# Kernel optimization log

Measured on AMD Instinct MI355X. Metric: run time of the kernel, lower is better.

## Reference

```python
import jax, jax.numpy as jnp
import numpy as np

OMEGA = 30.0
B = 65536
NUM_FREQ = 8  # int(base_dim / in_features) = 32 / 4


def _siren_w(k, out_dim, in_dim, first=False):
    bound = (1.0 / in_dim) if first else (np.sqrt(6.0 / in_dim) / OMEGA)
    return jax.random.uniform(k, (out_dim, in_dim), jnp.float32, -bound, bound)


def _lin_w(k, out_dim, in_dim):
    bound = np.sqrt(1.0 / in_dim)
    return jax.random.uniform(k, (out_dim, in_dim), jnp.float32, -bound, bound)


def setup_inputs() -> dict:
    key = jax.random.key(0)
    ks = jax.random.split(key, 16)
    E = 7
    d = {}
    d['x'] = jax.random.uniform(ks[0], (B, 4), jnp.float32, -1.0, 1.0)
    # encoder: pos_dim=64 -> sine1(128) -> sine2(256) -> resblock(256, bottleneck 128)
    d['enc_s1_w'] = _siren_w(ks[1], 128, 64, first=True); d['enc_s1_b'] = jnp.zeros((128,), jnp.float32)
    d['enc_s2_w'] = _siren_w(ks[2], 256, 128); d['enc_s2_b'] = jnp.zeros((256,), jnp.float32)
    d['res_fc1_w'] = _lin_w(ks[3], 128, 256); d['res_fc1_b'] = jnp.zeros((128,), jnp.float32)
    d['res_fc2_w'] = _lin_w(ks[4], 128, 128); d['res_fc2_b'] = jnp.zeros((128,), jnp.float32)
    d['res_fc3_w'] = _lin_w(ks[5], 256, 128); d['res_fc3_b'] = jnp.zeros((256,), jnp.float32)
    # policy: 4 -> 128 (first sine) -> 128 (sine); gate in = 256+128=384 -> 7
    d['pol_s1_w'] = _siren_w(ks[6], 128, 4, first=True); d['pol_s1_b'] = jnp.zeros((128,), jnp.float32)
    d['pol_s2_w'] = _siren_w(ks[7], 128, 128); d['pol_s2_b'] = jnp.zeros((128,), jnp.float32)
    d['gate_w'] = _siren_w(ks[8], 7, 384); d['gate_b'] = jnp.zeros((7,), jnp.float32)
    # 7 experts: SirenMLP 256 -> 256 (first sine) -> 256 (sine) -> final Linear 256 -> 1
    bnd1 = 1.0 / 256.0
    d['exp_s1_w'] = jax.random.uniform(ks[9], (E, 256, 256), jnp.float32, -bnd1, bnd1)
    d['exp_s1_b'] = jnp.zeros((E, 256), jnp.float32)
    bnd2 = np.sqrt(6.0 / 256.0) / OMEGA
    d['exp_s2_w'] = jax.random.uniform(ks[10], (E, 256, 256), jnp.float32, -bnd2, bnd2)
    d['exp_s2_b'] = jnp.zeros((E, 256), jnp.float32)
    d['exp_fin_w'] = jax.random.uniform(ks[11], (E, 1, 256), jnp.float32, -bnd2, bnd2)
    d['exp_fin_b'] = jnp.zeros((E, 1), jnp.float32)
    return d


def reference(x, enc_s1_w, enc_s1_b, enc_s2_w, enc_s2_b, res_fc1_w, res_fc1_b,
              res_fc2_w, res_fc2_b, res_fc3_w, res_fc3_b, pol_s1_w, pol_s1_b,
              pol_s2_w, pol_s2_b, gate_w, gate_b, exp_s1_w, exp_s1_b,
              exp_s2_w, exp_s2_b, exp_fin_w, exp_fin_b):
    # NeRF-style positional encoding: log-sampled freqs, no include_input
    freqs = (2.0 ** jnp.arange(NUM_FREQ, dtype=jnp.float32)) * jnp.pi  # [F]
    ang = x[:, :, None] * freqs                                        # [B,4,F]
    pe = jnp.concatenate([jnp.sin(ang), jnp.cos(ang)], axis=-1)        # [B,4,2F]
    pe = pe.reshape(x.shape[0], -1)                                    # [B,64]
    # shared encoder: sine1 -> sine2 -> bottleneck res block
    h = jnp.sin(OMEGA * (pe @ enc_s1_w.T + enc_s1_b))                  # [B,128]
    h = jnp.sin(OMEGA * (h @ enc_s2_w.T + enc_s2_b))                   # [B,256]
    r = jax.nn.relu(h @ res_fc1_w.T + res_fc1_b)                       # [B,128]
    r = jax.nn.relu(r @ res_fc2_w.T + res_fc2_b)                       # [B,128]
    r = r @ res_fc3_w.T + res_fc3_b                                    # [B,256]
    enc_feat = jax.nn.relu(r + h)                                      # [B,256]
    # policy: sine feature net + gate over [enc_feat, pol_feat]
    pf = jnp.sin(OMEGA * (x @ pol_s1_w.T + pol_s1_b))                  # [B,128]
    pf = jnp.sin(OMEGA * (pf @ pol_s2_w.T + pol_s2_b))                 # [B,128]
    logits = jnp.concatenate([enc_feat, pf], axis=-1) @ gate_w.T + gate_b  # [B,7]
    probs = jax.nn.softmax(logits, axis=-1)                            # [B,7]
    # all 7 expert SIREN MLPs as batched GEMMs over expert axis e
    e = jnp.sin(OMEGA * (jnp.einsum('bd,eod->beo', enc_feat, exp_s1_w) + exp_s1_b))  # [B,7,256]
    e = jnp.sin(OMEGA * (jnp.einsum('beh,eoh->beo', e, exp_s2_w) + exp_s2_b))        # [B,7,256]
    preds = jnp.einsum('beh,eoh->beo', e, exp_fin_w) + exp_fin_b                     # [B,7,1]
    # soft routing: probability-weighted combination
    y = jnp.sum(preds * probs[:, :, None], axis=1)                     # [B,1]
    return y
```

## Files before the change

### kernel.cpp

```cpp
#include <hip/hip_runtime.h>


typedef short v8s __attribute__((ext_vector_type(8)));
typedef float v4f __attribute__((ext_vector_type(4)));

#define KSIN 4.774648293f
#define AST 264
#define PST 9
#define N_CVT 8

__device__ __forceinline__ float bf2f(unsigned short h) {
  union { unsigned u; float f; } v; v.u = ((unsigned)h) << 16; return v.f;
}
__device__ __forceinline__ unsigned short f2bf(float f) {
  union { float f; unsigned u; } v; v.f = f;
  unsigned r = v.u + 0x7fffu + ((v.u >> 16) & 1u);
  return (unsigned short)(r >> 16);
}
__device__ __forceinline__ unsigned pack2(float a, float b) {
  return (unsigned)f2bf(a) | ((unsigned)f2bf(b) << 16);
}
__device__ __forceinline__ float sin_rev(float x) {
  return __builtin_amdgcn_sinf(x);
}
__device__ __forceinline__ float cos_rev(float x) {
  return __builtin_amdgcn_cosf(x);
}

struct CvtArgs {
  const float* src[N_CVT];
  unsigned     off[N_CVT];
  unsigned     n[N_CVT];
  float        scl[N_CVT];
};

__global__ void convert_kernel(CvtArgs a, unsigned short* __restrict__ dst) {
  const int tid = blockIdx.x * blockDim.x + threadIdx.x;
  const int stride = gridDim.x * blockDim.x;
  for (int k = 0; k < N_CVT; k++) {
    const unsigned n4 = a.n[k] >> 2;
    const float4* s = (const float4*)a.src[k];
    const float sc = a.scl[k];
    uint2* d = (uint2*)(dst + a.off[k]);
    for (unsigned i = tid; i < n4; i += stride) {
      float4 v = s[i];
      uint2 o; o.x = pack2(v.x * sc, v.y * sc); o.y = pack2(v.z * sc, v.w * sc);
      d[i] = o;
    }
    for (unsigned i = (n4 << 2) + tid; i < a.n[k]; i += stride)
      dst[a.off[k] + i] = f2bf(a.src[k][i] * sc);
  }
}

template<int K, int NPW, int ACT>
__device__ __forceinline__ void wgemm(const unsigned short* A,
                                      unsigned short* OUT, int oc,
                                      const unsigned short* __restrict__ W,
                                      const float* __restrict__ bias,
                                      const unsigned short* skip) {
  const int lane = threadIdx.x & 63;
  const int wave = threadIdx.x >> 6;
  const int m15  = lane & 15;
  const int q    = lane >> 4;
  const int n0   = wave * (NPW * 16);
  v4f acc[NPW][4];
#pragma unroll
  for (int i = 0; i < NPW; i++)
#pragma unroll
    for (int j = 0; j < 4; j++) acc[i][j] = (v4f){0.f, 0.f, 0.f, 0.f};

#pragma unroll
  for (int k0 = 0; k0 < K / 32; ++k0) {
    v8s a[4], b[NPW];
#pragma unroll
    for (int rt = 0; rt < 4; rt++)
      a[rt] = *(const v8s*)(A + (rt * 16 + m15) * AST + k0 * 32 + q * 8);
#pragma unroll
    for (int ct = 0; ct < NPW; ct++)
      b[ct] = *(const v8s*)(W + (size_t)(n0 + ct * 16 + m15) * K + k0 * 32 + q * 8);
#pragma unroll
    for (int ct = 0; ct < NPW; ct++)
#pragma unroll
      for (int rt = 0; rt < 4; rt++)
        acc[ct][rt] = __builtin_amdgcn_mfma_f32_16x16x32_bf16(b[ct], a[rt], acc[ct][rt], 0, 0, 0);
  }

#pragma unroll
  for (int ct = 0; ct < NPW; ct++) {
    const int c0 = n0 + ct * 16 + q * 4;
    v4f bv = *(const v4f*)(bias + c0);
    if (ACT == 0) bv *= KSIN;
#pragma unroll
    for (int rt = 0; rt < 4; rt++) {
      const int row = rt * 16 + m15;
      float o0, o1, o2, o3;
      if (ACT == 2) {
        const uint2 sk = *(const uint2*)(skip + row * AST + c0);
        o0 = fmaxf(acc[ct][rt][0] + bv[0] + bf2f((unsigned short)(sk.x & 0xffffu)), 0.f);
        o1 = fmaxf(acc[ct][rt][1] + bv[1] + bf2f((unsigned short)(sk.x >> 16)), 0.f);
        o2 = fmaxf(acc[ct][rt][2] + bv[2] + bf2f((unsigned short)(sk.y & 0xffffu)), 0.f);
        o3 = fmaxf(acc[ct][rt][3] + bv[3] + bf2f((unsigned short)(sk.y >> 16)), 0.f);
      } else if (ACT == 1) {
        o0 = fmaxf(acc[ct][rt][0] + bv[0], 0.f);
        o1 = fmaxf(acc[ct][rt][1] + bv[1], 0.f);
        o2 = fmaxf(acc[ct][rt][2] + bv[2], 0.f);
        o3 = fmaxf(acc[ct][rt][3] + bv[3], 0.f);
      } else {
        o0 = sin_rev(acc[ct][rt][0] + bv[0]);
        o1 = sin_rev(acc[ct][rt][1] + bv[1]);
        o2 = sin_rev(acc[ct][rt][2] + bv[2]);
        o3 = sin_rev(acc[ct][rt][3] + bv[3]);
      }
      uint2 w2; w2.x = pack2(o0, o1); w2.y = pack2(o2, o3);
      *(uint2*)(OUT + row * AST + oc + c0) = w2;
    }
  }
}

__device__ __forceinline__ void wexpert2(const unsigned short* A,
                                         const unsigned short* __restrict__ W,
                                         const float* __restrict__ bias,
                                         const float* __restrict__ wfin,
                                         float* __restrict__ pred_part) {
  const int lane = threadIdx.x & 63;
  const int wave = threadIdx.x >> 6;
  const int m15  = lane & 15;
  const int q    = lane >> 4;
  const int n0   = wave * 32;
  v4f acc[2][4];
#pragma unroll
  for (int i = 0; i < 2; i++)
#pragma unroll
    for (int j = 0; j < 4; j++) acc[i][j] = (v4f){0.f, 0.f, 0.f, 0.f};

#pragma unroll
  for (int k0 = 0; k0 < 8; ++k0) {
    v8s a[4], b[2];
#pragma unroll
    for (int rt = 0; rt < 4; rt++)
      a[rt] = *(const v8s*)(A + (rt * 16 + m15) * AST + k0 * 32 + q * 8);
#pragma unroll
    for (int ct = 0; ct < 2; ct++)
      b[ct] = *(const v8s*)(W + (size_t)(n0 + ct * 16 + m15) * 256 + k0 * 32 + q * 8);
#pragma unroll
    for (int ct = 0; ct < 2; ct++)
#pragma unroll
      for (int rt = 0; rt < 4; rt++)
        acc[ct][rt] = __builtin_amdgcn_mfma_f32_16x16x32_bf16(b[ct], a[rt], acc[ct][rt], 0, 0, 0);
  }

  float p[4] = {0.f, 0.f, 0.f, 0.f};
#pragma unroll
  for (int ct = 0; ct < 2; ct++) {
    const int c0 = n0 + ct * 16 + q * 4;
    v4f bv = *(const v4f*)(bias + c0);
    bv *= KSIN;
    const v4f wf = *(const v4f*)(wfin + c0);
#pragma unroll
    for (int rt = 0; rt < 4; rt++)
#pragma unroll
      for (int r = 0; r < 4; r++)
        p[rt] += sin_rev(acc[ct][rt][r] + bv[r]) * wf[r];
  }
#pragma unroll
  for (int rt = 0; rt < 4; rt++) {
    float v = p[rt];
    v += __shfl_xor(v, 16);
    v += __shfl_xor(v, 32);
    if (q == 0) pred_part[wave * 64 + rt * 16 + m15] = v;
  }
}

__global__ __launch_bounds__(512, 2) void moe_inr_kernel(
    const float* __restrict__ x,
    const unsigned short* __restrict__ es1w, const float* __restrict__ es1b,
    const unsigned short* __restrict__ es2w, const float* __restrict__ es2b,
    const unsigned short* __restrict__ rf1w, const float* __restrict__ rf1b,
    const unsigned short* __restrict__ rf2w, const float* __restrict__ rf2b,
    const unsigned short* __restrict__ rf3w, const float* __restrict__ rf3b,
    const float* __restrict__ ps1w,          const float* __restrict__ ps1b,
    const unsigned short* __restrict__ ps2w, const float* __restrict__ ps2b,
    const float* __restrict__ gw,            const float* __restrict__ gb,
    const unsigned short* __restrict__ xs1w, const float* __restrict__ xs1b,
    const unsigned short* __restrict__ xs2w, const float* __restrict__ xs2b,
    const float* __restrict__ xfw,           const float* __restrict__ xfb,
    float* __restrict__ out) {
  __shared__ __align__(16) unsigned short P[2][64 * AST];
  __shared__ __align__(16) unsigned short Q[2][64 * AST];
  __shared__ float probs[2][64 * PST];
  __shared__ float pred_part[2][8 * 64];

  const int t   = threadIdx.x;
  const int r0g = blockIdx.x * 128;

#pragma unroll
  for (int tl = 0; tl < 2; ++tl) {
    const int row = t & 63, g = t >> 6, c = g & 3, jh = g >> 2;
    const float xv = x[(r0g + tl * 64 + row) * 4 + c];
    float sn[4], cs[4];
#pragma unroll
    for (int jj = 0; jj < 4; jj++) {
      const int j = jh * 4 + jj;
      const float rev = xv * (0.5f * (float)(1 << j));
      sn[jj] = sin_rev(rev);
      cs[jj] = cos_rev(rev);
    }
    uint2 ws; ws.x = pack2(sn[0], sn[1]); ws.y = pack2(sn[2], sn[3]);
    uint2 wc2; wc2.x = pack2(cs[0], cs[1]); wc2.y = pack2(cs[2], cs[3]);
    *(uint2*)(P[tl] + row * AST + c * 16 + jh * 4) = ws;
    *(uint2*)(P[tl] + row * AST + c * 16 + 8 + jh * 4) = wc2;
  }
  __syncthreads();
  wgemm<64, 1, 0>(P[0], P[0], 64, es1w, es1b, nullptr);
  wgemm<64, 1, 0>(P[1], P[1], 64, es1w, es1b, nullptr);
  __syncthreads();
  wgemm<128, 2, 0>(P[0] + 64, Q[0], 0, es2w, es2b, nullptr);
  wgemm<128, 2, 0>(P[1] + 64, Q[1], 0, es2w, es2b, nullptr);
  __syncthreads();
  wgemm<256, 1, 1>(Q[0], P[0], 0, rf1w, rf1b, nullptr);
  wgemm<256, 1, 1>(Q[1], P[1], 0, rf1w, rf1b, nullptr);
  __syncthreads();
  wgemm<128, 1, 1>(P[0], P[0], 128, rf2w, rf2b, nullptr);
  wgemm<128, 1, 1>(P[1], P[1], 128, rf2w, rf2b, nullptr);
  __syncthreads();
  wgemm<128, 2, 2>(P[0] + 128, Q[0], 0, rf3w, rf3b, Q[0]);
  wgemm<128, 2, 2>(P[1] + 128, Q[1], 0, rf3w, rf3b, Q[1]);
  __syncthreads();
#pragma unroll
  for (int tl = 0; tl < 2; ++tl) {
    const int row = t & 63, g = t >> 6;
    const v4f xv = *(const v4f*)(x + (r0g + tl * 64 + row) * 4);
#pragma unroll
    for (int ii = 0; ii < 4; ii++) {
      float oo[4];
#pragma unroll
      for (int i2 = 0; i2 < 4; i2++) {
        const int o = g * 16 + ii * 4 + i2;
        const v4f w4 = *(const v4f*)(ps1w + o * 4);
        const float z = xv[0] * w4[0] + xv[1] * w4[1] + xv[2] * w4[2] +
                        xv[3] * w4[3] + ps1b[o];
        oo[i2] = sin_rev(KSIN * z);
      }
      uint2 w2; w2.x = pack2(oo[0], oo[1]); w2.y = pack2(oo[2], oo[3]);
      *(uint2*)(P[tl] + row * AST + g * 16 + ii * 4) = w2;
    }
  }
  __syncthreads();
  wgemm<128, 1, 0>(P[0], P[0], 128, ps2w, ps2b, nullptr);
  wgemm<128, 1, 0>(P[1], P[1], 128, ps2w, ps2b, nullptr);
  __syncthreads();
#pragma unroll
  for (int tl = 0; tl < 2; ++tl) {
    const int row = t >> 3, pp = t & 7;
    float lg[7] = {0.f, 0.f, 0.f, 0.f, 0.f, 0.f, 0.f};
#pragma unroll
    for (int u = 0; u < 6; u++) {
      const int kk = pp * 48 + u * 8;
      const v8s av = (kk < 256) ? *(const v8s*)(Q[tl] + row * AST + kk)
                                : *(const v8s*)(P[tl] + row * AST + 128 + (kk - 256));
      float af[8];
#pragma unroll
      for (int e2 = 0; e2 < 8; e2++) af[e2] = bf2f((unsigned short)av[e2]);
#pragma unroll
      for (int j = 0; j < 7; j++) {
        const v4f g0 = *(const v4f*)(gw + j * 384 + kk);
        const v4f g1 = *(const v4f*)(gw + j * 384 + kk + 4);
        lg[j] += af[0] * g0[0] + af[1] * g0[1] + af[2] * g0[2] + af[3] * g0[3] +
                 af[4] * g1[0] + af[5] * g1[1] + af[6] * g1[2] + af[7] * g1[3];
      }
    }
#pragma unroll
    for (int j = 0; j < 7; j++) {
      float s = lg[j];
      s += __shfl_xor(s, 1);
      s += __shfl_xor(s, 2);
      s += __shfl_xor(s, 4);
      lg[j] = s;
    }
    if (pp == 0) {
#pragma unroll
      for (int j = 0; j < 7; j++) probs[tl][row * PST + j] = lg[j] + gb[j];
    }
  }
  __syncthreads();
  float yr = 0.f;
  if (t < 128) {
    const int tl = t >> 6, row = t & 63;
    float m = probs[tl][row * PST];
#pragma unroll
    for (int j = 1; j < 7; j++) m = fmaxf(m, probs[tl][row * PST + j]);
    float s = 0.f, e[7];
#pragma unroll
    for (int j = 0; j < 7; j++) { e[j] = __expf(probs[tl][row * PST + j] - m); s += e[j]; }
    const float inv = 1.f / s;
#pragma unroll
    for (int j = 0; j < 7; j++) probs[tl][row * PST + j] = e[j] * inv;
  }
  for (int ex = 0; ex < 7; ++ex) {
    wgemm<256, 2, 0>(Q[0], P[0], 0, xs1w + ex * 65536, xs1b + ex * 256, nullptr);
    wgemm<256, 2, 0>(Q[1], P[1], 0, xs1w + ex * 65536, xs1b + ex * 256, nullptr);
    __syncthreads();
    wexpert2(P[0], xs2w + ex * 65536, xs2b + ex * 256, xfw + ex * 256, pred_part[0]);
    wexpert2(P[1], xs2w + ex * 65536, xs2b + ex * 256, xfw + ex * 256, pred_part[1]);
    __syncthreads();
    if (t < 128) {
      const int tl = t >> 6, row = t & 63;
      float pr = 0.f;
#pragma unroll
      for (int w = 0; w < 8; w++) pr += pred_part[tl][w * 64 + row];
      yr += (pr + xfb[ex]) * probs[tl][row * PST + ex];
    }
  }
  if (t < 128) out[r0g + t] = yr;
}

extern "C" void kernel_launch(void* const* d_in, const int* in_sizes, int n_in,
                              void* d_out, int out_size, void* d_ws, size_t ws_size,
                              hipStream_t stream) {
  (void)out_size; (void)n_in; (void)ws_size;
  const int   idx[N_CVT] = {1, 3, 5, 7, 9, 13, 17, 19};
  const float scl[N_CVT] = {KSIN, KSIN, 1.f, 1.f, 1.f, KSIN, KSIN, KSIN};
  unsigned off[N_CVT], cur = 0;
  CvtArgs a;
  for (int i = 0; i < N_CVT; i++) {
    off[i] = cur;
    a.src[i] = (const float*)d_in[idx[i]];
    a.off[i] = cur;
    a.n[i]   = (unsigned)in_sizes[idx[i]];
    a.scl[i] = scl[i];
    cur += ((unsigned)in_sizes[idx[i]] + 7u) & ~7u;
  }
  unsigned short* dst = (unsigned short*)d_ws;
  hipLaunchKernelGGL(convert_kernel, dim3(1024), dim3(256), 0, stream, a, dst);
  hipLaunchKernelGGL(moe_inr_kernel, dim3(65536 / 128), dim3(512), 0, stream,
      (const float*)d_in[0],
      dst + off[0], (const float*)d_in[2],
      dst + off[1], (const float*)d_in[4],
      dst + off[2], (const float*)d_in[6],
      dst + off[3], (const float*)d_in[8],
      dst + off[4], (const float*)d_in[10],
      (const float*)d_in[11], (const float*)d_in[12],
      dst + off[5], (const float*)d_in[14],
      (const float*)d_in[15], (const float*)d_in[16],
      dst + off[6], (const float*)d_in[18],
      dst + off[7], (const float*)d_in[20],
      (const float*)d_in[21], (const float*)d_in[22],
      (float*)d_out);
}
```

Before: 350.3 us.

## Split waves across the two row tiles instead of looping tiles per wave

Each GEMM stage now assigns half the waves (4 of 8) to each 64-row tile, with every wave covering twice as many output columns, instead of every wave processing both tiles one after the other. Each wave loads its weight fragments once and reuses them across 4 column tiles, which cuts global weight traffic per wave and removes the serial tile loop. In exchange each wave holds more accumulator registers (up to 16 v4f), which raises register pressure under the 512x2 launch bounds and may cause spills.

```diff
diff --git a/kernel.cpp b/kernel.cpp
--- a/kernel.cpp
+++ b/kernel.cpp
@@ -53,16 +53,24 @@
 }
 
 template<int K, int NPW, int ACT>
-__device__ __forceinline__ void wgemm(const unsigned short* A,
-                                      unsigned short* OUT, int oc,
-                                      const unsigned short* __restrict__ W,
-                                      const float* __restrict__ bias,
-                                      const unsigned short* skip) {
+__device__ __forceinline__ void wgemm1(const unsigned short* A0,
+                                       const unsigned short* A1,
+                                       unsigned short* O0, unsigned short* O1,
+                                       int oc,
+                                       const unsigned short* __restrict__ W,
+                                       const float* __restrict__ bias,
+                                       const unsigned short* skip0,
+                                       const unsigned short* skip1) {
   const int lane = threadIdx.x & 63;
   const int wave = threadIdx.x >> 6;
+  const int tl   = wave >> 2;
+  const int wl   = wave & 3;
   const int m15  = lane & 15;
   const int q    = lane >> 4;
-  const int n0   = wave * (NPW * 16);
+  const int n0   = wl * (NPW * 16);
+  const unsigned short* A   = tl ? A1 : A0;
+  unsigned short*       OUT = tl ? O1 : O0;
+  const unsigned short* skp = tl ? skip1 : skip0;
   v4f acc[NPW][4];
 #pragma unroll
   for (int i = 0; i < NPW; i++)
@@ -73,11 +81,11 @@
   for (int k0 = 0; k0 < K / 32; ++k0) {
     v8s a[4], b[NPW];
 #pragma unroll
+    for (int ct = 0; ct < NPW; ct++)
+      b[ct] = *(const v8s*)(W + (size_t)(n0 + ct * 16 + m15) * K + k0 * 32 + q * 8);
+#pragma unroll
     for (int rt = 0; rt < 4; rt++)
       a[rt] = *(const v8s*)(A + (rt * 16 + m15) * AST + k0 * 32 + q * 8);
-#pragma unroll
-    for (int ct = 0; ct < NPW; ct++)
-      b[ct] = *(const v8s*)(W + (size_t)(n0 + ct * 16 + m15) * K + k0 * 32 + q * 8);
 #pragma unroll
     for (int ct = 0; ct < NPW; ct++)
 #pragma unroll
@@ -93,23 +101,24 @@
 #pragma unroll
     for (int rt = 0; rt < 4; rt++) {
       const int row = rt * 16 + m15;
+      const v4f av = acc[ct][rt];
       float o0, o1, o2, o3;
       if (ACT == 2) {
-        const uint2 sk = *(const uint2*)(skip + row * AST + c0);
-        o0 = fmaxf(acc[ct][rt][0] + bv[0] + bf2f((unsigned short)(sk.x & 0xffffu)), 0.f);
-        o1 = fmaxf(acc[ct][rt][1] + bv[1] + bf2f((unsigned short)(sk.x >> 16)), 0.f);
-        o2 = fmaxf(acc[ct][rt][2] + bv[2] + bf2f((unsigned short)(sk.y & 0xffffu)), 0.f);
-        o3 = fmaxf(acc[ct][rt][3] + bv[3] + bf2f((unsigned short)(sk.y >> 16)), 0.f);
+        const uint2 sk = *(const uint2*)(skp + row * AST + c0);
+        o0 = fmaxf(av[0] + bv[0] + bf2f((unsigned short)(sk.x & 0xffffu)), 0.f);
+        o1 = fmaxf(av[1] + bv[1] + bf2f((unsigned short)(sk.x >> 16)), 0.f);
+        o2 = fmaxf(av[2] + bv[2] + bf2f((unsigned short)(sk.y & 0xffffu)), 0.f);
+        o3 = fmaxf(av[3] + bv[3] + bf2f((unsigned short)(sk.y >> 16)), 0.f);
       } else if (ACT == 1) {
-        o0 = fmaxf(acc[ct][rt][0] + bv[0], 0.f);
-        o1 = fmaxf(acc[ct][rt][1] + bv[1], 0.f);
-        o2 = fmaxf(acc[ct][rt][2] + bv[2], 0.f);
-        o3 = fmaxf(acc[ct][rt][3] + bv[3], 0.f);
+        o0 = fmaxf(av[0] + bv[0], 0.f);
+        o1 = fmaxf(av[1] + bv[1], 0.f);
+        o2 = fmaxf(av[2] + bv[2], 0.f);
+        o3 = fmaxf(av[3] + bv[3], 0.f);
       } else {
-        o0 = sin_rev(acc[ct][rt][0] + bv[0]);
-        o1 = sin_rev(acc[ct][rt][1] + bv[1]);
-        o2 = sin_rev(acc[ct][rt][2] + bv[2]);
-        o3 = sin_rev(acc[ct][rt][3] + bv[3]);
+        o0 = sin_rev(av[0] + bv[0]);
+        o1 = sin_rev(av[1] + bv[1]);
+        o2 = sin_rev(av[2] + bv[2]);
+        o3 = sin_rev(av[3] + bv[3]);
       }
       uint2 w2; w2.x = pack2(o0, o1); w2.y = pack2(o2, o3);
       *(uint2*)(OUT + row * AST + oc + c0) = w2;
@@ -117,33 +126,37 @@
   }
 }
 
-__device__ __forceinline__ void wexpert2(const unsigned short* A,
-                                         const unsigned short* __restrict__ W,
-                                         const float* __restrict__ bias,
-                                         const float* __restrict__ wfin,
-                                         float* __restrict__ pred_part) {
+__device__ __forceinline__ void wexpert2s(const unsigned short* A0,
+                                          const unsigned short* A1,
+                                          const unsigned short* __restrict__ W,
+                                          const float* __restrict__ bias,
+                                          const float* __restrict__ wfin,
+                                          float* __restrict__ pp) {
   const int lane = threadIdx.x & 63;
   const int wave = threadIdx.x >> 6;
+  const int tl   = wave >> 2;
+  const int wl   = wave & 3;
   const int m15  = lane & 15;
   const int q    = lane >> 4;
-  const int n0   = wave * 32;
-  v4f acc[2][4];
-#pragma unroll
-  for (int i = 0; i < 2; i++)
+  const int n0   = wl * 64;
+  const unsigned short* A = tl ? A1 : A0;
+  v4f acc[4][4];
+#pragma unroll
+  for (int i = 0; i < 4; i++)
 #pragma unroll
     for (int j = 0; j < 4; j++) acc[i][j] = (v4f){0.f, 0.f, 0.f, 0.f};
 
 #pragma unroll
   for (int k0 = 0; k0 < 8; ++k0) {
-    v8s a[4], b[2];
+    v8s a[4], b[4];
+#pragma unroll
+    for (int ct = 0; ct < 4; ct++)
+      b[ct] = *(const v8s*)(W + (size_t)(n0 + ct * 16 + m15) * 256 + k0 * 32 + q * 8);
 #pragma unroll
     for (int rt = 0; rt < 4; rt++)
       a[rt] = *(const v8s*)(A + (rt * 16 + m15) * AST + k0 * 32 + q * 8);
 #pragma unroll
-    for (int ct = 0; ct < 2; ct++)
-      b[ct] = *(const v8s*)(W + (size_t)(n0 + ct * 16 + m15) * 256 + k0 * 32 + q * 8);
-#pragma unroll
-    for (int ct = 0; ct < 2; ct++)
+    for (int ct = 0; ct < 4; ct++)
 #pragma unroll
       for (int rt = 0; rt < 4; rt++)
         acc[ct][rt] = __builtin_amdgcn_mfma_f32_16x16x32_bf16(b[ct], a[rt], acc[ct][rt], 0, 0, 0);
@@ -151,7 +164,7 @@
 
   float p[4] = {0.f, 0.f, 0.f, 0.f};
 #pragma unroll
-  for (int ct = 0; ct < 2; ct++) {
+  for (int ct = 0; ct < 4; ct++) {
     const int c0 = n0 + ct * 16 + q * 4;
     v4f bv = *(const v4f*)(bias + c0);
     bv *= KSIN;
@@ -167,7 +180,7 @@
     float v = p[rt];
     v += __shfl_xor(v, 16);
     v += __shfl_xor(v, 32);
-    if (q == 0) pred_part[wave * 64 + rt * 16 + m15] = v;
+    if (q == 0) pp[tl * 256 + wl * 64 + rt * 16 + m15] = v;
   }
 }
 
@@ -188,7 +201,7 @@
   __shared__ __align__(16) unsigned short P[2][64 * AST];
   __shared__ __align__(16) unsigned short Q[2][64 * AST];
   __shared__ float probs[2][64 * PST];
-  __shared__ float pred_part[2][8 * 64];
+  __shared__ float pred_part[2 * 4 * 64];
 
   const int t   = threadIdx.x;
   const int r0g = blockIdx.x * 128;
@@ -211,20 +224,15 @@
     *(uint2*)(P[tl] + row * AST + c * 16 + 8 + jh * 4) = wc2;
   }
   __syncthreads();
-  wgemm<64, 1, 0>(P[0], P[0], 64, es1w, es1b, nullptr);
-  wgemm<64, 1, 0>(P[1], P[1], 64, es1w, es1b, nullptr);
-  __syncthreads();
-  wgemm<128, 2, 0>(P[0] + 64, Q[0], 0, es2w, es2b, nullptr);
-  wgemm<128, 2, 0>(P[1] + 64, Q[1], 0, es2w, es2b, nullptr);
-  __syncthreads();
-  wgemm<256, 1, 1>(Q[0], P[0], 0, rf1w, rf1b, nullptr);
-  wgemm<256, 1, 1>(Q[1], P[1], 0, rf1w, rf1b, nullptr);
-  __syncthreads();
-  wgemm<128, 1, 1>(P[0], P[0], 128, rf2w, rf2b, nullptr);
-  wgemm<128, 1, 1>(P[1], P[1], 128, rf2w, rf2b, nullptr);
-  __syncthreads();
-  wgemm<128, 2, 2>(P[0] + 128, Q[0], 0, rf3w, rf3b, Q[0]);
-  wgemm<128, 2, 2>(P[1] + 128, Q[1], 0, rf3w, rf3b, Q[1]);
+  wgemm1<64, 2, 0>(P[0], P[1], P[0], P[1], 64, es1w, es1b, nullptr, nullptr);
+  __syncthreads();
+  wgemm1<128, 4, 0>(P[0] + 64, P[1] + 64, Q[0], Q[1], 0, es2w, es2b, nullptr, nullptr);
+  __syncthreads();
+  wgemm1<256, 2, 1>(Q[0], Q[1], P[0], P[1], 0, rf1w, rf1b, nullptr, nullptr);
+  __syncthreads();
+  wgemm1<128, 2, 1>(P[0], P[1], P[0], P[1], 128, rf2w, rf2b, nullptr, nullptr);
+  __syncthreads();
+  wgemm1<128, 4, 2>(P[0] + 128, P[1] + 128, Q[0], Q[1], 0, rf3w, rf3b, Q[0], Q[1]);
   __syncthreads();
 #pragma unroll
   for (int tl = 0; tl < 2; ++tl) {
@@ -246,8 +254,7 @@
     }
   }
   __syncthreads();
-  wgemm<128, 1, 0>(P[0], P[0], 128, ps2w, ps2b, nullptr);
-  wgemm<128, 1, 0>(P[1], P[1], 128, ps2w, ps2b, nullptr);
+  wgemm1<128, 2, 0>(P[0], P[1], P[0], P[1], 128, ps2w, ps2b, nullptr, nullptr);
   __syncthreads();
 #pragma unroll
   for (int tl = 0; tl < 2; ++tl) {
@@ -297,17 +304,16 @@
     for (int j = 0; j < 7; j++) probs[tl][row * PST + j] = e[j] * inv;
   }
   for (int ex = 0; ex < 7; ++ex) {
-    wgemm<256, 2, 0>(Q[0], P[0], 0, xs1w + ex * 65536, xs1b + ex * 256, nullptr);
-    wgemm<256, 2, 0>(Q[1], P[1], 0, xs1w + ex * 65536, xs1b + ex * 256, nullptr);
+    wgemm1<256, 4, 0>(Q[0], Q[1], P[0], P[1], 0,
+                      xs1w + ex * 65536, xs1b + ex * 256, nullptr, nullptr);
     __syncthreads();
-    wexpert2(P[0], xs2w + ex * 65536, xs2b + ex * 256, xfw + ex * 256, pred_part[0]);
-    wexpert2(P[1], xs2w + ex * 65536, xs2b + ex * 256, xfw + ex * 256, pred_part[1]);
+    wexpert2s(P[0], P[1], xs2w + ex * 65536, xs2b + ex * 256, xfw + ex * 256,
+              pred_part);
     __syncthreads();
     if (t < 128) {
       const int tl = t >> 6, row = t & 63;
-      float pr = 0.f;
-#pragma unroll
-      for (int w = 0; w < 8; w++) pr += pred_part[tl][w * 64 + row];
+      float pr = pred_part[tl * 256 + row] + pred_part[tl * 256 + 64 + row] +
+                 pred_part[tl * 256 + 128 + row] + pred_part[tl * 256 + 192 + row];
       yr += (pr + xfb[ex]) * probs[tl][row * PST + ex];
     }
   }
```

After: 433.4 us. 1.24x slower.
